# Performance work log

Measured on AMD Instinct MI355X. Metric: run time of the kernel, lower is better.

Reference implementation:

```python
import jax, jax.numpy as jnp
import numpy as np

N_NODES = 100000
N_EDGES = 1600000
D_IN = 128
HID = 128
N_GRAPHS = 500
NODES_PER_GRAPH = N_NODES // N_GRAPHS


def setup_inputs() -> dict:
    key = jax.random.key(0)
    k1, k2, k3, k4 = jax.random.split(key, 4)
    x = jax.random.normal(k1, (N_NODES, D_IN), dtype=jnp.float32)
    edge_index = jax.random.randint(k2, (2, N_EDGES), 0, N_NODES, dtype=jnp.int64)
    scope = jnp.full((N_GRAPHS,), NODES_PER_GRAPH, dtype=jnp.int64)  # sums to N_NODES
    W1 = jax.random.normal(k3, (D_IN, HID), dtype=jnp.float32) * 0.05
    b1 = jnp.zeros((HID,), dtype=jnp.float32)
    W2 = jax.random.normal(k4, (HID, HID), dtype=jnp.float32) * 0.05
    b2 = jnp.zeros((HID,), dtype=jnp.float32)
    return {"x": x, "edge_index": edge_index, "scope": scope,
            "W1": W1, "b1": b1, "W2": W2, "b2": b2}


def gcn_conv(x, src, dst, W, b, n_nodes):
    # PyG GCNConv: add self loops, symmetric normalization D^-1/2 (A+I) D^-1/2,
    # then linear transform and scatter-add aggregation at target nodes.
    h = x @ W  # [N, H]
    loop = jnp.arange(n_nodes, dtype=src.dtype)
    s = jnp.concatenate([src, loop])
    d = jnp.concatenate([dst, loop])
    ones = jnp.ones(s.shape[0], dtype=h.dtype)
    deg = jax.ops.segment_sum(ones, d, num_segments=n_nodes)  # >=1 due to self loops
    dinv = jax.lax.rsqrt(deg)
    norm = dinv[s] * dinv[d]  # [E+N]
    msgs = h[s] * norm[:, None]  # gather + scale, memory bound
    out = jax.ops.segment_sum(msgs, d, num_segments=n_nodes)  # scatter-add
    return out + b


def reference(x, edge_index, scope, W1, b1, W2, b2):
    src, dst = edge_index[0], edge_index[1]
    h = gcn_conv(x, src, dst, W1, b1, N_NODES)
    # NOTE: original calls self.bn1(h) but discards the result; dropout is
    # identity in eval mode, so only ReLU applies between the two convs.
    h = jax.nn.relu(h)
    h2 = gcn_conv(h, src, dst, W2, b2, N_NODES)
    # ragged per-graph mean pooling (torch.split + mean + stack)
    seg = jnp.repeat(jnp.arange(N_GRAPHS), scope, total_repeat_length=N_NODES)
    sums = jax.ops.segment_sum(h2, seg, num_segments=N_GRAPHS)  # [G, H]
    return sums / scope[:, None].astype(h2.dtype)
```

## Files before the change

### kernel.cpp

```cpp
#include <hip/hip_runtime.h>
#include <hip/hip_bf16.h>
#include <stdint.h>

#define NN 100000
#define NE 1600000
#define HD 128
#define NG 500
#define NPG 200

#define NBK 782
#define NBLK 128
#define CHUNK 12500

typedef __attribute__((ext_vector_type(8))) short short8v;
typedef __attribute__((ext_vector_type(4))) float float4v;
typedef __attribute__((ext_vector_type(2))) float float2v;

__device__ __forceinline__ float bflo(unsigned int u) { return __uint_as_float(u << 16); }
__device__ __forceinline__ float bfhi(unsigned int u) { return __uint_as_float(u & 0xffff0000u); }
__device__ __forceinline__ unsigned int packbf(float a, float b) {
  unsigned int ua = __float_as_uint(a), ub = __float_as_uint(b);
  ua += 0x7fffu + ((ua >> 16) & 1u);
  ub += 0x7fffu + ((ub >> 16) & 1u);
  return (ua >> 16) | (ub & 0xffff0000u);
}

__device__ __forceinline__ int edge_at(const void* p, int is64, int idx) {
  return is64 ? (int)((const long long*)p)[idx] : ((const int*)p)[idx];
}

__device__ __forceinline__ int detect_is64(const void* edges, int tid, int* sf) {
  if (tid == 0) *sf = 0;
  __syncthreads();
  const unsigned int* p = (const unsigned int*)edges;
  unsigned int e = p[2 * tid], o = p[2 * tid + 1];
  unsigned int m = (e ? 1u : 0u) | (o ? 2u : 0u);
  if (m) atomicOr(sf, (int)m);
  __syncthreads();
  int v = *sf;
  return ((v & 2) == 0) && (v & 1);
}

__global__ __launch_bounds__(256) void k_hist1(const void* __restrict__ edges,
                                               int* __restrict__ hist) {
  __shared__ int lh[1024];
  __shared__ int sf;
  int tid = threadIdx.x, blk = blockIdx.x;
  int f = detect_is64(edges, tid, &sf);
  for (int i = tid; i < NBK; i += 256) lh[i] = 0;
  __syncthreads();
  int e0 = blk * CHUNK, e1 = e0 + CHUNK;
  if (e1 > NE) e1 = NE;
  for (int e = e0 + tid; e < e1; e += 256) {
    int d = edge_at(edges, f, NE + e);
    atomicAdd(&lh[d >> 7], 1);
  }
  __syncthreads();
  for (int i = tid; i < NBK; i += 256) hist[i * NBLK + blk] = lh[i];
}

__global__ void k_scan_block(const int* __restrict__ in, int* __restrict__ outv,
                             int* __restrict__ bsums, int n) {
  __shared__ int s[256];
  int tid = threadIdx.x;
  int i = blockIdx.x * 256 + tid;
  int v = (i < n) ? in[i] : 0;
  s[tid] = v;
  __syncthreads();
  for (int off = 1; off < 256; off <<= 1) {
    int t = (tid >= off) ? s[tid - off] : 0;
    __syncthreads();
    s[tid] += t;
    __syncthreads();
  }
  if (i < n) outv[i] = s[tid] - v;
  if (tid == 255) bsums[blockIdx.x] = s[255];
}

__global__ void k_scan_sums(int* __restrict__ bsums, int nb) {
  __shared__ int s[512];
  int tid = threadIdx.x;
  int v = (tid < nb) ? bsums[tid] : 0;
  s[tid] = v;
  __syncthreads();
  for (int off = 1; off < 512; off <<= 1) {
    int t = (tid >= off) ? s[tid - off] : 0;
    __syncthreads();
    s[tid] += t;
    __syncthreads();
  }
  if (tid < nb) bsums[tid] = s[tid] - v;
}

__global__ void k_scan_add(int* __restrict__ outv, const int* __restrict__ bsums, int n) {
  int i = blockIdx.x * blockDim.x + threadIdx.x;
  if (i < n) outv[i] += bsums[i >> 8];
}

__global__ __launch_bounds__(256) void k_scatter(const void* __restrict__ edges,
                                                 const int* __restrict__ histS,
                                                 unsigned int* __restrict__ sorted) {
  __shared__ int base[1024];
  __shared__ int sf;
  int tid = threadIdx.x, blk = blockIdx.x;
  int f = detect_is64(edges, tid, &sf);
  for (int i = tid; i < NBK; i += 256) base[i] = histS[i * NBLK + blk];
  __syncthreads();
  int e0 = blk * CHUNK, e1 = e0 + CHUNK;
  if (e1 > NE) e1 = NE;
  for (int e = e0 + tid; e < e1; e += 256) {
    int s = edge_at(edges, f, e);
    int d = edge_at(edges, f, NE + e);
    int pos = atomicAdd(&base[d >> 7], 1);
    sorted[pos] = ((unsigned)(d & 127) << 17) | (unsigned)s;
  }
}

__global__ __launch_bounds__(256) void k_passB2(const unsigned int* __restrict__ sorted,
                                                const int* __restrict__ histS,
                                                int* __restrict__ rowstart,
                                                float* __restrict__ dinv,
                                                int* __restrict__ csr) {
  __shared__ int cnt[128];
  __shared__ int sc[256];
  __shared__ int fill[128];
  __shared__ int stage[4096];
  int b = blockIdx.x, tid = threadIdx.x;
  int ebase = histS[b * NBLK];
  int eend = (b + 1 < NBK) ? histS[(b + 1) * NBLK] : NE;
  int ne = eend - ebase;
  if (tid < 128) { cnt[tid] = 0; fill[tid] = 0; }
  __syncthreads();
  for (int i = tid; i < ne; i += 256) {
    unsigned int r = sorted[ebase + i];
    atomicAdd(&cnt[r >> 17], 1);
  }
  __syncthreads();
  int v = (tid < 128) ? cnt[tid] : 0;
  sc[tid] = v;
  __syncthreads();
  for (int off = 1; off < 256; off <<= 1) {
    int t = (tid >= off) ? sc[tid - off] : 0;
    __syncthreads();
    sc[tid] += t;
    __syncthreads();
  }
  int node = (b << 7) + tid;
  if (tid < 128 && node < NN) {
    rowstart[node] = ebase + sc[tid] - cnt[tid];
    dinv[node] = rsqrtf((float)(cnt[tid] + 1));
  }
  if (b == NBK - 1 && tid == 0) rowstart[NN] = NE;
  __syncthreads();
  for (int i = tid; i < ne; i += 256) {
    unsigned int r = sorted[ebase + i];
    int ld = (int)(r >> 17);
    int pos = atomicAdd(&fill[ld], 1);
    stage[sc[ld] - cnt[ld] + pos] = (int)(r & 0x1FFFFu);
  }
  __syncthreads();
  for (int i = tid; i < ne; i += 256) csr[ebase + i] = stage[i];
}

__global__ __launch_bounds__(256) void k_order(const int* __restrict__ rowstart,
                                               int* __restrict__ order) {
  __shared__ int h[128];
  __shared__ int sc[256];
  __shared__ int fill[128];
  __shared__ int degs[256];
  int g = blockIdx.x, tid = threadIdx.x;
  if (tid < 128) { h[tid] = 0; fill[tid] = 0; }
  __syncthreads();
  if (tid < NPG) {
    int n = g * NPG + tid;
    int d = rowstart[n + 1] - rowstart[n];
    if (d > 127) d = 127;
    degs[tid] = d;
    atomicAdd(&h[d], 1);
  }
  __syncthreads();
  int v = (tid < 128) ? h[tid] : 0;
  sc[tid] = v;
  __syncthreads();
  for (int off = 1; off < 256; off <<= 1) {
    int t = (tid >= off) ? sc[tid - off] : 0;
    __syncthreads();
    sc[tid] += t;
    __syncthreads();
  }
  if (tid < NPG) {
    int d = degs[tid];
    int pos = sc[d] - h[d] + atomicAdd(&fill[d], 1);
    order[g * NPG + pos] = g * NPG + tid;
  }
}

__global__ void k_cvt8(const float4* __restrict__ in, uint2* __restrict__ out,
                       const float* __restrict__ dinv) {
  int i = blockIdx.x * 256 + threadIdx.x;
  float s = dinv[i >> 4] * 8.f;
  float4 a = in[(size_t)i * 2], b = in[(size_t)i * 2 + 1];
  int w0 = __builtin_amdgcn_cvt_pk_fp8_f32(a.x * s, a.y * s, 0, false);
  w0 = __builtin_amdgcn_cvt_pk_fp8_f32(a.z * s, a.w * s, w0, true);
  int w1 = __builtin_amdgcn_cvt_pk_fp8_f32(b.x * s, b.y * s, 0, false);
  w1 = __builtin_amdgcn_cvt_pk_fp8_f32(b.z * s, b.w * s, w1, true);
  out[i] = make_uint2((unsigned)w0, (unsigned)w1);
}

__global__ void k_cvtW(const float* __restrict__ W, unsigned int* __restrict__ Wt) {
  int i = blockIdx.x * 256 + threadIdx.x;
  int c = i >> 6, kp = i & 63;
  float w0 = W[(size_t)(2 * kp) * 128 + c];
  float w1 = W[(size_t)(2 * kp + 1) * 128 + c];
  Wt[c * 64 + kp] = packbf(w0, w1);
}

__device__ __forceinline__ void accf8(float* a, uint2 v) {
  float2v f;
  f = __builtin_amdgcn_cvt_pk_f32_fp8((int)v.x, false); a[0] += f.x; a[1] += f.y;
  f = __builtin_amdgcn_cvt_pk_f32_fp8((int)v.x, true);  a[2] += f.x; a[3] += f.y;
  f = __builtin_amdgcn_cvt_pk_f32_fp8((int)v.y, false); a[4] += f.x; a[5] += f.y;
  f = __builtin_amdgcn_cvt_pk_f32_fp8((int)v.y, true);  a[6] += f.x; a[7] += f.y;
}

#define AGG_CORE8(IN, NODE, L, A)                                                \
  float A[8] = {0.f, 0.f, 0.f, 0.f, 0.f, 0.f, 0.f, 0.f};                         \
  {                                                                              \
    uint2 sv = IN[(size_t)(NODE)*16 + (L)];                                      \
    accf8(A, sv);                                                                \
  }                                                                              \
  {                                                                              \
    int i = rowstart[NODE], end = rowstart[(NODE) + 1];                          \
    for (; i + 7 < end; i += 8) {                                                \
      int s0 = csr[i], s1 = csr[i + 1], s2 = csr[i + 2], s3 = csr[i + 3];        \
      int s4 = csr[i + 4], s5 = csr[i + 5], s6 = csr[i + 6], s7 = csr[i + 7];    \
      uint2 v0 = IN[(size_t)s0 * 16 + (L)];                                      \
      uint2 v1 = IN[(size_t)s1 * 16 + (L)];                                      \
      uint2 v2 = IN[(size_t)s2 * 16 + (L)];                                      \
      uint2 v3 = IN[(size_t)s3 * 16 + (L)];                                      \
      uint2 v4 = IN[(size_t)s4 * 16 + (L)];                                      \
      uint2 v5 = IN[(size_t)s5 * 16 + (L)];                                      \
      uint2 v6 = IN[(size_t)s6 * 16 + (L)];                                      \
      uint2 v7 = IN[(size_t)s7 * 16 + (L)];                                      \
      accf8(A, v0); accf8(A, v1); accf8(A, v2); accf8(A, v3);                    \
      accf8(A, v4); accf8(A, v5); accf8(A, v6); accf8(A, v7);                    \
    }                                                                            \
    for (; i + 3 < end; i += 4) {                                                \
      int s0 = csr[i], s1 = csr[i + 1], s2 = csr[i + 2], s3 = csr[i + 3];        \
      uint2 v0 = IN[(size_t)s0 * 16 + (L)];                                      \
      uint2 v1 = IN[(size_t)s1 * 16 + (L)];                                      \
      uint2 v2 = IN[(size_t)s2 * 16 + (L)];                                      \
      uint2 v3 = IN[(size_t)s3 * 16 + (L)];                                      \
      accf8(A, v0); accf8(A, v1); accf8(A, v2); accf8(A, v3);                    \
    }                                                                            \
    for (; i < end; ++i) {                                                       \
      uint2 v0 = IN[(size_t)csr[i] * 16 + (L)];                                  \
      accf8(A, v0);                                                              \
    }                                                                            \
  }

__global__ __launch_bounds__(256) void k_agg1g(const uint2* __restrict__ in,
                                               const unsigned int* __restrict__ W1t,
                                               const float* __restrict__ bias,
                                               uint2* __restrict__ out,
                                               const int* __restrict__ rowstart,
                                               const int* __restrict__ csr,
                                               const float* __restrict__ dinv,
                                               const int* __restrict__ order) {
  __shared__ uint4 At[16 * 16];
  __shared__ float Ot[16 * 128];
  __shared__ float sdv[16];
  int tid = threadIdx.x;
  int qw = tid >> 4, l = tid & 15;
  int pos = blockIdx.x * 16 + qw;
  int node = order[pos];
  AGG_CORE8(in, node, l, a)
  float dv = dinv[node];
  if (l == 0) sdv[qw] = dv;
  {
    float ds = dv * 0.125f;
    uint4 o;
    o.x = packbf(a[0] * ds, a[1] * ds); o.y = packbf(a[2] * ds, a[3] * ds);
    o.z = packbf(a[4] * ds, a[5] * ds); o.w = packbf(a[6] * ds, a[7] * ds);
    At[qw * 16 + (l ^ (qw & 7))] = o;
  }
  __syncthreads();

  int w = tid >> 6, lane = tid & 63;
  int m = lane & 15, g = lane >> 4;
  float4v acc[2];
  acc[0] = (float4v)0.f;
  acc[1] = (float4v)0.f;
#pragma unroll
  for (int ks = 0; ks < 4; ++ks) {
    int slot = ks * 4 + g;
    short8v af = *(const short8v*)&At[m * 16 + (slot ^ (m & 7))];
#pragma unroll
    for (int t = 0; t < 2; ++t) {
      int c = (w * 2 + t) * 16 + m;
      short8v bf = *(const short8v*)&W1t[c * 64 + ks * 16 + g * 4];
      acc[t] = __builtin_amdgcn_mfma_f32_16x16x32_bf16(af, bf, acc[t], 0, 0, 0);
    }
  }
#pragma unroll
  for (int t = 0; t < 2; ++t) {
    int c = (w * 2 + t) * 16 + m;
    float bl = bias[c];
#pragma unroll
    for (int j = 0; j < 4; ++j) {
      int r = g * 4 + j;
      float v = fmaxf(acc[t][j] + bl, 0.f) * (sdv[r] * 16.f);
      *(float*)((char*)Ot + r * 512 + ((c * 4) ^ ((r & 7) << 4))) = v;
    }
  }
  __syncthreads();
  {
    int s = (qw & 7) << 4;
    const char* base = (const char*)Ot + qw * 512;
    float4 f0 = *(const float4*)(base + ((l * 32) ^ s));
    float4 f1 = *(const float4*)(base + ((l * 32 + 16) ^ s));
    int w0 = __builtin_amdgcn_cvt_pk_fp8_f32(f0.x, f0.y, 0, false);
    w0 = __builtin_amdgcn_cvt_pk_fp8_f32(f0.z, f0.w, w0, true);
    int w1 = __builtin_amdgcn_cvt_pk_fp8_f32(f1.x, f1.y, 0, false);
    w1 = __builtin_amdgcn_cvt_pk_fp8_f32(f1.z, f1.w, w1, true);
    out[(size_t)node * 16 + l] = make_uint2((unsigned)w0, (unsigned)w1);
  }
}

__global__ __launch_bounds__(256) void k_agg2p(const uint2* __restrict__ in,
                                               float* __restrict__ poolsum,
                                               const int* __restrict__ rowstart,
                                               const int* __restrict__ csr,
                                               const float* __restrict__ dinv,
                                               const int* __restrict__ order) {
  __shared__ float sh[16][128];
  int nl = threadIdx.x >> 4, l = threadIdx.x & 15;
  int pos = blockIdx.x * 16 + nl;
  int node = order[pos];
  AGG_CORE8(in, node, l, a)
  float dv = dinv[node];
#pragma unroll
  for (int j = 0; j < 8; ++j) a[j] *= dv;
  *(float4*)&sh[nl][l * 8] = make_float4(a[0], a[1], a[2], a[3]);
  *(float4*)&sh[nl][l * 8 + 4] = make_float4(a[4], a[5], a[6], a[7]);
  __syncthreads();
  int tid = threadIdx.x;
  if (tid < 128) {
    int n0 = blockIdx.x * 16;
    int gA = n0 / NPG;
    int split = (gA + 1) * NPG - n0;
    if (split > 16) split = 16;
    float sA = 0.f, sB = 0.f;
#pragma unroll
    for (int n = 0; n < 16; ++n) {
      float v = sh[n][tid];
      if (n < split) sA += v; else sB += v;
    }
    atomicAdd(&poolsum[gA * 128 + tid], sA);
    if (split < 16) atomicAdd(&poolsum[(gA + 1) * 128 + tid], sB);
  }
}

__global__ __launch_bounds__(256) void k_gemm2s(const float* __restrict__ A,
                                                const float* __restrict__ W,
                                                const float* __restrict__ bias,
                                                float* __restrict__ out, int M, float ascale) {
  __shared__ float As[8][128];
  int tid = threadIdx.x;
  int row0 = blockIdx.x * 8;
  {
    int r = tid >> 5, c4 = (tid & 31) * 4;
    float4 v = make_float4(0.f, 0.f, 0.f, 0.f);
    if (row0 + r < M) v = *(const float4*)&A[(size_t)(row0 + r) * 128 + c4];
    *(float4*)&As[r][c4] = make_float4(v.x * ascale, v.y * ascale, v.z * ascale, v.w * ascale);
  }
  __syncthreads();
  int r = tid >> 5, c0 = (tid & 31) * 4;
  float acc0 = 0.f, acc1 = 0.f, acc2 = 0.f, acc3 = 0.f;
  for (int k = 0; k < 128; ++k) {
    float a = As[r][k];
    float4 wv = *(const float4*)&W[(size_t)k * 128 + c0];
    acc0 = fmaf(a, wv.x, acc0); acc1 = fmaf(a, wv.y, acc1);
    acc2 = fmaf(a, wv.z, acc2); acc3 = fmaf(a, wv.w, acc3);
  }
  if (row0 + r < M) {
    float4 o;
    o.x = acc0 + bias[c0]; o.y = acc1 + bias[c0 + 1];
    o.z = acc2 + bias[c0 + 2]; o.w = acc3 + bias[c0 + 3];
    *(float4*)&out[(size_t)(row0 + r) * 128 + c0] = o;
  }
}

extern "C" void kernel_launch(void* const* d_in, const int* in_sizes, int n_in,
                              void* d_out, int out_size, void* d_ws, size_t ws_size,
                              hipStream_t stream) {
  const float* x  = (const float*)d_in[0];
  const void* edges = d_in[1];
  const float* W1 = (const float*)d_in[3];
  const float* b1 = (const float*)d_in[4];
  const float* W2 = (const float*)d_in[5];
  const float* b2 = (const float*)d_in[6];
  float* out = (float*)d_out;

  char* ws = (char*)d_ws;
  float* poolsum  = (float*)(ws + 0);
  int*   hist     = (int*)(ws + 256000);
  int*   histS    = (int*)(ws + 656384);
  int*   bsums    = (int*)(ws + 1056768);
  int*   rowstart = (int*)(ws + 1058816);
  float* dinv     = (float*)(ws + 1458832);
  int*   order    = (int*)(ws + 1858832);
  unsigned int* W1t = (unsigned int*)(ws + 2258832);
  unsigned int* sorted = (unsigned int*)(ws + 2291600);
  int*   csr      = (int*)(ws + 8691600);
  void*  xs8      = (void*)(ws + 15091600);
  void*  h1s8     = (void*)(ws + 27891600);

  hipMemsetAsync(poolsum, 0, 256000, stream);

  const int NH = NBK * NBLK;

  k_hist1<<<NBLK, 256, 0, stream>>>(edges, hist);
  k_scan_block<<<(NH + 255) / 256, 256, 0, stream>>>(hist, histS, bsums, NH);
  k_scan_sums<<<1, 512, 0, stream>>>(bsums, (NH + 255) / 256);
  k_scan_add<<<(NH + 255) / 256, 256, 0, stream>>>(histS, bsums, NH);
  k_scatter<<<NBLK, 256, 0, stream>>>(edges, histS, sorted);
  k_passB2<<<NBK, 256, 0, stream>>>(sorted, histS, rowstart, dinv, csr);
  k_order<<<NG, 256, 0, stream>>>(rowstart, order);

  k_cvt8<<<NN * HD / 8 / 256, 256, 0, stream>>>((const float4*)x, (uint2*)xs8, dinv);
  k_cvtW<<<32, 256, 0, stream>>>(W1, W1t);

  k_agg1g<<<NN / 16, 256, 0, stream>>>((const uint2*)xs8, W1t, b1, (uint2*)h1s8,
                                       rowstart, csr, dinv, order);
  k_agg2p<<<NN / 16, 256, 0, stream>>>((const uint2*)h1s8, poolsum, rowstart, csr, dinv, order);
  k_gemm2s<<<(NG + 7) / 8, 256, 0, stream>>>(poolsum, W2, b2, out, NG, 1.f / 3200.f);
}
```

Baseline: 206.1 us.

## Bucket CSR neighbors by source quarter, fuse scan-add, reverse degree order

Within each destination row, neighbor indices are now sub-sorted into four source-index quarters, and per-row quarter counts are recorded in a packed rowquad array. Aggregation walks the four runs separately, so gathers across the wavefront and block tend to hit the same quarter of the feature table at the same time, which aims for better cache locality. The separate scan-add kernel is removed by adding block sums inline in scatter and passB2. The int64 edge read now loads only the low 32-bit word, the per-graph node order is reversed so high-degree nodes are scheduled first, and agg_run is shared between the two aggregation kernels. This adds extra LDS counters, more loop-tail overhead from four short runs, and an extra rowquad load per node.

```diff
diff --git a/kernel.cpp b/kernel.cpp
--- a/kernel.cpp
+++ b/kernel.cpp
@@ -25,8 +25,9 @@
   return (ua >> 16) | (ub & 0xffff0000u);
 }
 
-__device__ __forceinline__ int edge_at(const void* p, int is64, int idx) {
-  return is64 ? (int)((const long long*)p)[idx] : ((const int*)p)[idx];
+__device__ __forceinline__ int edge32(const void* p, int is64, int idx) {
+  const int* q = (const int*)p;
+  return is64 ? q[2 * idx] : q[idx];
 }
 
 __device__ __forceinline__ int detect_is64(const void* edges, int tid, int* sf) {
@@ -52,7 +53,7 @@
   int e0 = blk * CHUNK, e1 = e0 + CHUNK;
   if (e1 > NE) e1 = NE;
   for (int e = e0 + tid; e < e1; e += 256) {
-    int d = edge_at(edges, f, NE + e);
+    int d = edge32(edges, f, NE + e);
     atomicAdd(&lh[d >> 7], 1);
   }
   __syncthreads();
@@ -92,25 +93,24 @@
   if (tid < nb) bsums[tid] = s[tid] - v;
 }
 
-__global__ void k_scan_add(int* __restrict__ outv, const int* __restrict__ bsums, int n) {
-  int i = blockIdx.x * blockDim.x + threadIdx.x;
-  if (i < n) outv[i] += bsums[i >> 8];
-}
-
 __global__ __launch_bounds__(256) void k_scatter(const void* __restrict__ edges,
                                                  const int* __restrict__ histS,
+                                                 const int* __restrict__ bsums,
                                                  unsigned int* __restrict__ sorted) {
   __shared__ int base[1024];
   __shared__ int sf;
   int tid = threadIdx.x, blk = blockIdx.x;
   int f = detect_is64(edges, tid, &sf);
-  for (int i = tid; i < NBK; i += 256) base[i] = histS[i * NBLK + blk];
+  for (int i = tid; i < NBK; i += 256) {
+    int idx = i * NBLK + blk;
+    base[i] = histS[idx] + bsums[idx >> 8];
+  }
   __syncthreads();
   int e0 = blk * CHUNK, e1 = e0 + CHUNK;
   if (e1 > NE) e1 = NE;
   for (int e = e0 + tid; e < e1; e += 256) {
-    int s = edge_at(edges, f, e);
-    int d = edge_at(edges, f, NE + e);
+    int s = edge32(edges, f, e);
+    int d = edge32(edges, f, NE + e);
     int pos = atomicAdd(&base[d >> 7], 1);
     sorted[pos] = ((unsigned)(d & 127) << 17) | (unsigned)s;
   }
@@ -118,26 +118,38 @@
 
 __global__ __launch_bounds__(256) void k_passB2(const unsigned int* __restrict__ sorted,
                                                 const int* __restrict__ histS,
+                                                const int* __restrict__ bsums,
                                                 int* __restrict__ rowstart,
+                                                unsigned int* __restrict__ rowquad,
                                                 float* __restrict__ dinv,
                                                 int* __restrict__ csr) {
-  __shared__ int cnt[128];
+  __shared__ int cnt[512];
+  __shared__ int scx[512];
+  __shared__ int fill[512];
   __shared__ int sc[256];
-  __shared__ int fill[128];
   __shared__ int stage[4096];
   int b = blockIdx.x, tid = threadIdx.x;
-  int ebase = histS[b * NBLK];
-  int eend = (b + 1 < NBK) ? histS[(b + 1) * NBLK] : NE;
+  int i0 = b * NBLK;
+  int ebase = histS[i0] + bsums[i0 >> 8];
+  int eend = NE;
+  if (b + 1 < NBK) {
+    int i1 = (b + 1) * NBLK;
+    eend = histS[i1] + bsums[i1 >> 8];
+  }
   int ne = eend - ebase;
-  if (tid < 128) { cnt[tid] = 0; fill[tid] = 0; }
+  cnt[tid] = 0; cnt[tid + 256] = 0;
+  fill[tid] = 0; fill[tid + 256] = 0;
   __syncthreads();
   for (int i = tid; i < ne; i += 256) {
     unsigned int r = sorted[ebase + i];
-    atomicAdd(&cnt[r >> 17], 1);
-  }
-  __syncthreads();
-  int v = (tid < 128) ? cnt[tid] : 0;
-  sc[tid] = v;
+    int src = (int)(r & 0x1FFFFu);
+    int q = (src >= 25000) + (src >= 50000) + (src >= 75000);
+    atomicAdd(&cnt[((r >> 17) << 2) + q], 1);
+  }
+  __syncthreads();
+  int v0 = cnt[2 * tid], v1 = cnt[2 * tid + 1];
+  int ps = v0 + v1;
+  sc[tid] = ps;
   __syncthreads();
   for (int off = 1; off < 256; off <<= 1) {
     int t = (tid >= off) ? sc[tid - off] : 0;
@@ -145,18 +157,27 @@
     sc[tid] += t;
     __syncthreads();
   }
+  int ex = sc[tid] - ps;
+  scx[2 * tid] = ex;
+  scx[2 * tid + 1] = ex + v0;
+  __syncthreads();
   int node = (b << 7) + tid;
   if (tid < 128 && node < NN) {
-    rowstart[node] = ebase + sc[tid] - cnt[tid];
-    dinv[node] = rsqrtf((float)(cnt[tid] + 1));
+    int c0 = cnt[4 * tid], c1 = cnt[4 * tid + 1], c2 = cnt[4 * tid + 2], c3 = cnt[4 * tid + 3];
+    int deg = c0 + c1 + c2 + c3;
+    rowstart[node] = ebase + scx[4 * tid];
+    rowquad[node] = (unsigned)c0 | ((unsigned)c1 << 10) | ((unsigned)c2 << 20);
+    dinv[node] = rsqrtf((float)(deg + 1));
   }
   if (b == NBK - 1 && tid == 0) rowstart[NN] = NE;
   __syncthreads();
   for (int i = tid; i < ne; i += 256) {
     unsigned int r = sorted[ebase + i];
-    int ld = (int)(r >> 17);
-    int pos = atomicAdd(&fill[ld], 1);
-    stage[sc[ld] - cnt[ld] + pos] = (int)(r & 0x1FFFFu);
+    int src = (int)(r & 0x1FFFFu);
+    int q = (src >= 25000) + (src >= 50000) + (src >= 75000);
+    int key = (int)((r >> 17) << 2) + q;
+    int pos = atomicAdd(&fill[key], 1);
+    stage[scx[key] + pos] = src;
   }
   __syncthreads();
   for (int i = tid; i < ne; i += 256) csr[ebase + i] = stage[i];
@@ -191,7 +212,7 @@
   if (tid < NPG) {
     int d = degs[tid];
     int pos = sc[d] - h[d] + atomicAdd(&fill[d], 1);
-    order[g * NPG + pos] = g * NPG + tid;
+    order[g * NPG + (NPG - 1 - pos)] = g * NPG + tid;
   }
 }
 
@@ -223,40 +244,51 @@
   f = __builtin_amdgcn_cvt_pk_f32_fp8((int)v.y, true);  a[6] += f.x; a[7] += f.y;
 }
 
+__device__ __forceinline__ void agg_run(const uint2* __restrict__ in,
+                                        const int* __restrict__ csr,
+                                        int L, int i, int end, float* a) {
+  for (; i + 7 < end; i += 8) {
+    int s0 = csr[i], s1 = csr[i + 1], s2 = csr[i + 2], s3 = csr[i + 3];
+    int s4 = csr[i + 4], s5 = csr[i + 5], s6 = csr[i + 6], s7 = csr[i + 7];
+    uint2 v0 = in[(size_t)s0 * 16 + L];
+    uint2 v1 = in[(size_t)s1 * 16 + L];
+    uint2 v2 = in[(size_t)s2 * 16 + L];
+    uint2 v3 = in[(size_t)s3 * 16 + L];
+    uint2 v4 = in[(size_t)s4 * 16 + L];
+    uint2 v5 = in[(size_t)s5 * 16 + L];
+    uint2 v6 = in[(size_t)s6 * 16 + L];
+    uint2 v7 = in[(size_t)s7 * 16 + L];
+    accf8(a, v0); accf8(a, v1); accf8(a, v2); accf8(a, v3);
+    accf8(a, v4); accf8(a, v5); accf8(a, v6); accf8(a, v7);
+  }
+  for (; i + 3 < end; i += 4) {
+    int s0 = csr[i], s1 = csr[i + 1], s2 = csr[i + 2], s3 = csr[i + 3];
+    uint2 v0 = in[(size_t)s0 * 16 + L];
+    uint2 v1 = in[(size_t)s1 * 16 + L];
+    uint2 v2 = in[(size_t)s2 * 16 + L];
+    uint2 v3 = in[(size_t)s3 * 16 + L];
+    accf8(a, v0); accf8(a, v1); accf8(a, v2); accf8(a, v3);
+  }
+  for (; i < end; ++i) {
+    uint2 v0 = in[(size_t)csr[i] * 16 + L];
+    accf8(a, v0);
+  }
+}
+
 #define AGG_CORE8(IN, NODE, L, A)                                                \
   float A[8] = {0.f, 0.f, 0.f, 0.f, 0.f, 0.f, 0.f, 0.f};                         \
+  accf8(A, IN[(size_t)(NODE)*16 + (L)]);                                         \
   {                                                                              \
-    uint2 sv = IN[(size_t)(NODE)*16 + (L)];                                      \
-    accf8(A, sv);                                                                \
-  }                                                                              \
-  {                                                                              \
-    int i = rowstart[NODE], end = rowstart[(NODE) + 1];                          \
-    for (; i + 7 < end; i += 8) {                                                \
-      int s0 = csr[i], s1 = csr[i + 1], s2 = csr[i + 2], s3 = csr[i + 3];        \
-      int s4 = csr[i + 4], s5 = csr[i + 5], s6 = csr[i + 6], s7 = csr[i + 7];    \
-      uint2 v0 = IN[(size_t)s0 * 16 + (L)];                                      \
-      uint2 v1 = IN[(size_t)s1 * 16 + (L)];                                      \
-      uint2 v2 = IN[(size_t)s2 * 16 + (L)];                                      \
-      uint2 v3 = IN[(size_t)s3 * 16 + (L)];                                      \
-      uint2 v4 = IN[(size_t)s4 * 16 + (L)];                                      \
-      uint2 v5 = IN[(size_t)s5 * 16 + (L)];                                      \
-      uint2 v6 = IN[(size_t)s6 * 16 + (L)];                                      \
-      uint2 v7 = IN[(size_t)s7 * 16 + (L)];                                      \
-      accf8(A, v0); accf8(A, v1); accf8(A, v2); accf8(A, v3);                    \
-      accf8(A, v4); accf8(A, v5); accf8(A, v6); accf8(A, v7);                    \
-    }                                                                            \
-    for (; i + 3 < end; i += 4) {                                                \
-      int s0 = csr[i], s1 = csr[i + 1], s2 = csr[i + 2], s3 = csr[i + 3];        \
-      uint2 v0 = IN[(size_t)s0 * 16 + (L)];                                      \
-      uint2 v1 = IN[(size_t)s1 * 16 + (L)];                                      \
-      uint2 v2 = IN[(size_t)s2 * 16 + (L)];                                      \
-      uint2 v3 = IN[(size_t)s3 * 16 + (L)];                                      \
-      accf8(A, v0); accf8(A, v1); accf8(A, v2); accf8(A, v3);                    \
-    }                                                                            \
-    for (; i < end; ++i) {                                                       \
-      uint2 v0 = IN[(size_t)csr[i] * 16 + (L)];                                  \
-      accf8(A, v0);                                                              \
-    }                                                                            \
+    int base = rowstart[NODE];                                                   \
+    int endT = rowstart[(NODE) + 1];                                             \
+    unsigned rq = rowquad[NODE];                                                 \
+    int o1 = (int)(rq & 1023u);                                                  \
+    int o2 = o1 + (int)((rq >> 10) & 1023u);                                     \
+    int o3 = o2 + (int)((rq >> 20) & 1023u);                                     \
+    agg_run(IN, csr, (L), base, base + o1, A);                                   \
+    agg_run(IN, csr, (L), base + o1, base + o2, A);                              \
+    agg_run(IN, csr, (L), base + o2, base + o3, A);                              \
+    agg_run(IN, csr, (L), base + o3, endT, A);                                   \
   }
 
 __global__ __launch_bounds__(256) void k_agg1g(const uint2* __restrict__ in,
@@ -264,6 +296,7 @@
                                                const float* __restrict__ bias,
                                                uint2* __restrict__ out,
                                                const int* __restrict__ rowstart,
+                                               const unsigned int* __restrict__ rowquad,
                                                const int* __restrict__ csr,
                                                const float* __restrict__ dinv,
                                                const int* __restrict__ order) {
@@ -330,6 +363,7 @@
 __global__ __launch_bounds__(256) void k_agg2p(const uint2* __restrict__ in,
                                                float* __restrict__ poolsum,
                                                const int* __restrict__ rowstart,
+                                               const unsigned int* __restrict__ rowquad,
                                                const int* __restrict__ csr,
                                                const float* __restrict__ dinv,
                                                const int* __restrict__ order) {
@@ -410,11 +444,12 @@
   int*   rowstart = (int*)(ws + 1058816);
   float* dinv     = (float*)(ws + 1458832);
   int*   order    = (int*)(ws + 1858832);
-  unsigned int* W1t = (unsigned int*)(ws + 2258832);
-  unsigned int* sorted = (unsigned int*)(ws + 2291600);
-  int*   csr      = (int*)(ws + 8691600);
-  void*  xs8      = (void*)(ws + 15091600);
-  void*  h1s8     = (void*)(ws + 27891600);
+  unsigned int* rowquad = (unsigned int*)(ws + 2258832);
+  unsigned int* W1t = (unsigned int*)(ws + 2658832);
+  unsigned int* sorted = (unsigned int*)(ws + 2691600);
+  int*   csr      = (int*)(ws + 9091600);
+  void*  xs8      = (void*)(ws + 15491600);
+  void*  h1s8     = (void*)(ws + 28291600);
 
   hipMemsetAsync(poolsum, 0, 256000, stream);
 
@@ -423,16 +458,16 @@
   k_hist1<<<NBLK, 256, 0, stream>>>(edges, hist);
   k_scan_block<<<(NH + 255) / 256, 256, 0, stream>>>(hist, histS, bsums, NH);
   k_scan_sums<<<1, 512, 0, stream>>>(bsums, (NH + 255) / 256);
-  k_scan_add<<<(NH + 255) / 256, 256, 0, stream>>>(histS, bsums, NH);
-  k_scatter<<<NBLK, 256, 0, stream>>>(edges, histS, sorted);
-  k_passB2<<<NBK, 256, 0, stream>>>(sorted, histS, rowstart, dinv, csr);
+  k_scatter<<<NBLK, 256, 0, stream>>>(edges, histS, bsums, sorted);
+  k_passB2<<<NBK, 256, 0, stream>>>(sorted, histS, bsums, rowstart, rowquad, dinv, csr);
   k_order<<<NG, 256, 0, stream>>>(rowstart, order);
 
   k_cvt8<<<NN * HD / 8 / 256, 256, 0, stream>>>((const float4*)x, (uint2*)xs8, dinv);
   k_cvtW<<<32, 256, 0, stream>>>(W1, W1t);
 
   k_agg1g<<<NN / 16, 256, 0, stream>>>((const uint2*)xs8, W1t, b1, (uint2*)h1s8,
-                                       rowstart, csr, dinv, order);
-  k_agg2p<<<NN / 16, 256, 0, stream>>>((const uint2*)h1s8, poolsum, rowstart, csr, dinv, order);
+                                       rowstart, rowquad, csr, dinv, order);
+  k_agg2p<<<NN / 16, 256, 0, stream>>>((const uint2*)h1s8, poolsum, rowstart, rowquad,
+                                       csr, dinv, order);
   k_gemm2s<<<(NG + 7) / 8, 256, 0, stream>>>(poolsum, W2, b2, out, NG, 1.f / 3200.f);
 }
```

New measurement: 256.3 us. +24.4%, slower.
